# Performance work log

Measured on AMD Instinct MI355X. Metric: run time of the kernel, lower is better.

The kernel has to match this reference:

```python
import jax, jax.numpy as jnp
import numpy as np

H = 51  # hidden size hardcoded in the module

def _lstm_cell(x, h, c, W_ih, W_hh, b_ih, b_hh):
    # PyTorch LSTMCell: gates ordered (i, f, g, o)
    z = x @ W_ih.T + h @ W_hh.T + b_ih + b_hh  # [B, 4H]
    i, f, g, o = jnp.split(z, 4, axis=-1)
    i = jax.nn.sigmoid(i)
    f = jax.nn.sigmoid(f)
    g = jnp.tanh(g)
    o = jax.nn.sigmoid(o)
    c_new = f * c + i * g
    h_new = o * jnp.tanh(c_new)
    return h_new, c_new

def setup_inputs() -> dict:
    key = jax.random.key(0)
    ks = jax.random.split(key, 12)
    B, T = 512, 512
    s = 1.0 / np.sqrt(H)  # PyTorch default init scale
    def u(k, shape):
        return jax.random.uniform(k, shape, jnp.float32, -s, s)
    return {
        "input": jax.random.normal(ks[0], (B, T), jnp.float32),
        "W_ih1": u(ks[1], (4 * H, 1)),
        "W_hh1": u(ks[2], (4 * H, H)),
        "b_ih1": u(ks[3], (4 * H,)),
        "b_hh1": u(ks[4], (4 * H,)),
        "W_ih2": u(ks[5], (4 * H, H)),
        "W_hh2": u(ks[6], (4 * H, H)),
        "b_ih2": u(ks[7], (4 * H,)),
        "b_hh2": u(ks[8], (4 * H,)),
        "W_lin": u(ks[9], (1, H)),
        "b_lin": u(ks[10], (1,)),
        "future": 0,
    }

def reference(input, W_ih1, W_hh1, b_ih1, b_hh1, W_ih2, W_hh2, b_ih2, b_hh2, W_lin, b_lin, future):
    B, T = input.shape
    h1 = jnp.zeros((B, H), input.dtype)
    c1 = jnp.zeros((B, H), input.dtype)
    h2 = jnp.zeros((B, H), input.dtype)
    c2 = jnp.zeros((B, H), input.dtype)

    def step(carry, x_t):
        h1, c1, h2, c2 = carry
        h1, c1 = _lstm_cell(x_t, h1, c1, W_ih1, W_hh1, b_ih1, b_hh1)
        h2, c2 = _lstm_cell(h1, h2, c2, W_ih2, W_hh2, b_ih2, b_hh2)
        out = h2 @ W_lin.T + b_lin  # [B, 1]
        return (h1, c1, h2, c2), out

    xs = jnp.transpose(input)[:, :, None]  # [T, B, 1]
    carry, outs = jax.lax.scan(step, (h1, c1, h2, c2), xs)
    outputs = jnp.transpose(outs[:, :, 0])  # [B, T]

    if future > 0:
        last = outs[-1]  # [B, 1]

        def fstep(carry, _):
            state, x = carry
            state, out = step(state, x)
            return (state, out), out

        _, fouts = jax.lax.scan(fstep, (carry, last), None, length=future)
        outputs = jnp.concatenate([outputs, jnp.transpose(fouts[:, :, 0])], axis=1)
    return outputs
```

## Files before the change

### kernel.cpp

```cpp
#include <hip/hip_runtime.h>

#define Hh 51
#define TT 512
#define MR 2
#define NBLK 256
#define BT 512
#define SHR 80
#define NIT 514
#define LOG2E 1.4426950408889634f

typedef _Float16 half8 __attribute__((ext_vector_type(8)));
typedef __attribute__((ext_vector_type(4))) float f32x4;

__device__ __forceinline__ float fexp2(float x){ return __builtin_amdgcn_exp2f(x); }
__device__ __forceinline__ float frcp(float x){ return __builtin_amdgcn_rcpf(x); }
__device__ __forceinline__ float sigm(float x){ return frcp(1.f + fexp2(-LOG2E*x)); }
__device__ __forceinline__ float ftanh(float x){ return 1.f - 2.f*frcp(1.f + fexp2(2.f*LOG2E*x)); }
__device__ __forceinline__ unsigned short h16bits(_Float16 h){
    union { _Float16 h; unsigned short u; } c; c.h = h; return c.u;
}
__device__ __forceinline__ unsigned packhl(float v){
    _Float16 hi = (_Float16)v;
    _Float16 lo = (_Float16)(v - (float)hi);
    return (unsigned)h16bits(hi) | ((unsigned)h16bits(lo) << 16);
}

#define MFMAH(a,b,c) __builtin_amdgcn_mfma_f32_16x16x32_f16(a,b,c,0,0,0)

__global__ __launch_bounds__(BT, 2) void lstm2_fold(
    const float* __restrict__ input,
    const float* __restrict__ W_ih1,
    const float* __restrict__ W_hh1,
    const float* __restrict__ b_ih1,
    const float* __restrict__ b_hh1,
    const float* __restrict__ W_ih2,
    const float* __restrict__ W_hh2,
    const float* __restrict__ b_ih2,
    const float* __restrict__ b_hh2,
    const float* __restrict__ W_lin,
    const float* __restrict__ b_lin,
    float* __restrict__ out)
{
    __shared__ unsigned xsp[(TT+1)*MR];
    __shared__ float ob[TT*MR];
    __shared__ __align__(16) _Float16 H1[2][16*SHR];
    __shared__ __align__(16) _Float16 H2[2][16*SHR];

    const int tid  = threadIdx.x;
    const int wv   = tid >> 6;
    const int lane = tid & 63;
    const int quad = lane >> 4;
    const int n16  = lane & 15;
    const int row0 = blockIdx.x * MR;
    const bool g1  = (wv < 4);
    const bool w3  = (wv == 3);
    const int  w   = g1 ? wv : (wv - 4);
    const int  l   = 13 * w + n16;
    const bool valid = (n16 <= 12) && (l < Hh);
    const bool liveA = ((n16 & 11) == 0);
    const bool updL  = (quad < MR) && valid;
    const bool xw    = (wv == 0) && (n16 == 0) && (quad < MR);
    const int  fo    = n16 * SHR + quad * 8;
    const int  ho    = (quad * 4) * SHR + l;

#pragma unroll
    for (int i = 0; i < MR; ++i) {
        int idx = i * BT + tid; int m = idx >> 9, t = idx & 511;
        xsp[t * MR + m] = packhl(input[(row0 + m) * TT + t]);
    }
    if (tid < MR) xsp[TT * MR + tid] = 0u;
    for (int i = tid; i < 2 * 16 * SHR / 2; i += BT) {
        ((int*)H1)[i] = 0; ((int*)H2)[i] = 0;
    }

    half8 z8 = {0,0,0,0,0,0,0,0};
    half8 B1[4][2];
    half8 B2[4][2], B3[4][2];
    half8 Bout[2];
    const f32x4 zc = (f32x4){0.f,0.f,0.f,0.f};
#pragma unroll
    for (int gt = 0; gt < 4; ++gt) {
        int jrow = gt * Hh + l;
        float bias = 0.f, wih = 0.f;
        if (valid) {
            bias = g1 ? (b_ih1[jrow] + b_hh1[jrow]) : (b_ih2[jrow] + b_hh2[jrow]);
            wih  = g1 ? W_ih1[jrow] : 0.f;
        }
        _Float16 bhi = (_Float16)bias;
        _Float16 blo = (_Float16)(bias - (float)bhi);
        _Float16 wih_h = (_Float16)wih;
#pragma unroll
        for (int kt = 0; kt < 2; ++kt) {
            B1[gt][kt] = z8; B2[gt][kt] = z8; B3[gt][kt] = z8;
#pragma unroll
            for (int jj = 0; jj < 8; ++jj) {
                int k = kt * 32 + quad * 8 + jj;
                if (valid) {
                    if (g1) {
                        if (k < Hh)       B1[gt][kt][jj] = (_Float16)W_hh1[jrow * Hh + k];
                        else if (k == 51) B1[gt][kt][jj] = bhi;
                        else if (k == 52 || k == 53) B1[gt][kt][jj] = wih_h;
                        else if (k == 54) B1[gt][kt][jj] = blo;
                    } else {
                        if (k < Hh) {
                            B2[gt][kt][jj] = (_Float16)W_ih2[jrow * Hh + k];
                            B3[gt][kt][jj] = (_Float16)W_hh2[jrow * Hh + k];
                        } else if (k == 51) B2[gt][kt][jj] = bhi;
                        else if (k == 54)   B2[gt][kt][jj] = blo;
                    }
                }
            }
        }
    }
    {
        float blf = b_lin[0];
        _Float16 blhi = (_Float16)blf;
        _Float16 bllo = (_Float16)(blf - (float)blhi);
#pragma unroll
        for (int kt = 0; kt < 2; ++kt) {
            Bout[kt] = z8;
#pragma unroll
            for (int jj = 0; jj < 8; ++jj) {
                int k = kt * 32 + quad * 8 + jj;
                if (w3 && n16 == 0) {
                    if (k < Hh)       Bout[kt][jj] = (_Float16)W_lin[k];
                    else if (k == 51) Bout[kt][jj] = blhi;
                    else if (k == 54) Bout[kt][jj] = bllo;
                }
            }
        }
    }
    float cst = 0.f;

    half8 f1a = z8, f1b = z8;
    half8 f2a = z8, f2b = z8;

    __syncthreads();
    if (tid < MR) {
        int r = tid * 4 * SHR;
        const unsigned one = (unsigned)h16bits((_Float16)1.0f);
#pragma unroll
        for (int p = 0; p < 2; ++p) {
            H1[p][r + 51] = (_Float16)1.0f;  H1[p][r + 54] = (_Float16)1.0f;
            H2[p][r + 51] = (_Float16)1.0f;  H2[p][r + 54] = (_Float16)1.0f;
        }
        *(unsigned*)&H1[1][r + 52] = xsp[tid];
        (void)one;
    }
    __syncthreads();

    auto stepfn = [&](int n, int pA, int pB) {
        if (g1) {
            if (w3 && n >= 2) {
                if (liveA) {
                    f2a = *(const half8*)&H2[pB][fo];
                    f2b = *(const half8*)&H2[pB][fo + 32];
                }
            }
            if (n < TT) {
                unsigned xn = xw ? xsp[(n + 1) * MR + quad] : 0u;
                if (liveA) {
                    f1a = *(const half8*)&H1[pA][fo];
                    f1b = *(const half8*)&H1[pA][fo + 32];
                }
                f32x4 ac[4];
#pragma unroll
                for (int gt = 0; gt < 4; ++gt) {
                    f32x4 a = MFMAH(f1a, B1[gt][0], zc);
                    a       = MFMAH(f1b, B1[gt][1], a);
                    ac[gt] = a;
                }
                if (updL) {
                    float ii = sigm(ac[0][0]), ff = sigm(ac[1][0]);
                    float gg = ftanh(ac[2][0]), oo = sigm(ac[3][0]);
                    cst = fmaf(ff, cst, ii * gg);
                    float h = oo * ftanh(cst);
                    H1[pB][ho] = (_Float16)h;
                }
                if (xw) *(unsigned*)&H1[pB][(quad * 4) * SHR + 52] = xn;
            }
            if (w3 && n >= 2) {
                f32x4 ao = MFMAH(f2a, Bout[0], zc);
                ao       = MFMAH(f2b, Bout[1], ao);
                if (n16 == 0 && quad < MR) ob[(n - 2) * MR + quad] = ao[0];
            }
        } else if (n >= 1 && n <= TT) {
            if (liveA) {
                f1a = *(const half8*)&H1[pA][fo];
                f1b = *(const half8*)&H1[pA][fo + 32];
                f2a = *(const half8*)&H2[pB][fo];
                f2b = *(const half8*)&H2[pB][fo + 32];
            }
            f32x4 ac[4];
#pragma unroll
            for (int gt = 0; gt < 4; ++gt) {
                f32x4 a = MFMAH(f2a, B3[gt][0], zc);
                a       = MFMAH(f2b, B3[gt][1], a);
                a       = MFMAH(f1a, B2[gt][0], a);
                a       = MFMAH(f1b, B2[gt][1], a);
                ac[gt] = a;
            }
            if (updL) {
                float ii = sigm(ac[0][0]), ff = sigm(ac[1][0]);
                float gg = ftanh(ac[2][0]), oo = sigm(ac[3][0]);
                cst = fmaf(ff, cst, ii * gg);
                float h = oo * ftanh(cst);
                H2[pA][ho] = (_Float16)h;
            }
        }
        __syncthreads();
    };

    for (int k2 = 0; k2 < NIT / 2; ++k2) {
        stepfn(2 * k2,     1, 0);
        stepfn(2 * k2 + 1, 0, 1);
    }

#pragma unroll
    for (int i = 0; i < MR; ++i) {
        int idx = i * BT + tid; int m = idx >> 9, t = idx & 511;
        out[(row0 + m) * TT + t] = ob[t * MR + m];
    }
}

extern "C" void kernel_launch(void* const* d_in, const int* in_sizes, int n_in,
                              void* d_out, int out_size, void* d_ws, size_t ws_size,
                              hipStream_t stream) {
    const float* input = (const float*)d_in[0];
    const float* W_ih1 = (const float*)d_in[1];
    const float* W_hh1 = (const float*)d_in[2];
    const float* b_ih1 = (const float*)d_in[3];
    const float* b_hh1 = (const float*)d_in[4];
    const float* W_ih2 = (const float*)d_in[5];
    const float* W_hh2 = (const float*)d_in[6];
    const float* b_ih2 = (const float*)d_in[7];
    const float* b_hh2 = (const float*)d_in[8];
    const float* W_lin = (const float*)d_in[9];
    const float* b_lin = (const float*)d_in[10];
    float* out = (float*)d_out;

    hipLaunchKernelGGL(lstm2_fold, dim3(NBLK), dim3(BT), 0, stream,
                       input, W_ih1, W_hh1, b_ih1, b_hh1,
                       W_ih2, W_hh2, b_ih2, b_hh2, W_lin, b_lin, out);
}
```

Baseline: 272.0 us.

## Deepen LSTM wavefront pipeline to four stages with split MFMA chains

Expands the shared hidden-state buffers from double to quad buffering and skews the schedule. The second layer's input-weight product on h1 is computed one step early from a prefetched copy, and the output projection is lagged an extra step. Long dependent MFMA accumulation chains are split into independent MFMAs whose results are summed in scalar registers, which shortens the per-step critical path between barriers. The cost is two extra pipeline iterations, more shared memory and more live registers, which may hurt occupancy under the 2-blocks-per-CU launch bound.

```diff
diff --git a/kernel.cpp b/kernel.cpp
--- a/kernel.cpp
+++ b/kernel.cpp
@@ -6,7 +6,7 @@
 #define NBLK 256
 #define BT 512
 #define SHR 80
-#define NIT 514
+#define NIT 516
 #define LOG2E 1.4426950408889634f
 
 typedef _Float16 half8 __attribute__((ext_vector_type(8)));
@@ -43,8 +43,8 @@
 {
     __shared__ unsigned xsp[(TT+1)*MR];
     __shared__ float ob[TT*MR];
-    __shared__ __align__(16) _Float16 H1[2][16*SHR];
-    __shared__ __align__(16) _Float16 H2[2][16*SHR];
+    __shared__ __align__(16) _Float16 H1[4][16*SHR];
+    __shared__ __align__(16) _Float16 H2[4][16*SHR];
 
     const int tid  = threadIdx.x;
     const int wv   = tid >> 6;
@@ -69,7 +69,7 @@
         xsp[t * MR + m] = packhl(input[(row0 + m) * TT + t]);
     }
     if (tid < MR) xsp[TT * MR + tid] = 0u;
-    for (int i = tid; i < 2 * 16 * SHR / 2; i += BT) {
+    for (int i = tid; i < 4 * 16 * SHR / 2; i += BT) {
         ((int*)H1)[i] = 0; ((int*)H2)[i] = 0;
     }
 
@@ -134,86 +134,109 @@
 
     half8 f1a = z8, f1b = z8;
     half8 f2a = z8, f2b = z8;
+    half8 pf1a = z8, pf1b = z8;
+    half8 of2a = z8, of2b = z8;
 
     __syncthreads();
     if (tid < MR) {
         int r = tid * 4 * SHR;
-        const unsigned one = (unsigned)h16bits((_Float16)1.0f);
-#pragma unroll
-        for (int p = 0; p < 2; ++p) {
+#pragma unroll
+        for (int p = 0; p < 4; ++p) {
             H1[p][r + 51] = (_Float16)1.0f;  H1[p][r + 54] = (_Float16)1.0f;
             H2[p][r + 51] = (_Float16)1.0f;  H2[p][r + 54] = (_Float16)1.0f;
         }
-        *(unsigned*)&H1[1][r + 52] = xsp[tid];
-        (void)one;
+        *(unsigned*)&H1[3][r + 52] = xsp[tid];
     }
     __syncthreads();
 
-    auto stepfn = [&](int n, int pA, int pB) {
+    auto stepfn = [&](int n, int P) {
+        const int Sr1 = (P + 3) & 3;
+        const int Sw1 = P;
+        const int Sr2 = (P + 1) & 3;
+        const int Sw2 = (P + 2) & 3;
         if (g1) {
-            if (w3 && n >= 2) {
-                if (liveA) {
-                    f2a = *(const half8*)&H2[pB][fo];
-                    f2b = *(const half8*)&H2[pB][fo + 32];
-                }
-            }
             if (n < TT) {
                 unsigned xn = xw ? xsp[(n + 1) * MR + quad] : 0u;
                 if (liveA) {
-                    f1a = *(const half8*)&H1[pA][fo];
-                    f1b = *(const half8*)&H1[pA][fo + 32];
-                }
-                f32x4 ac[4];
+                    f1a = *(const half8*)&H1[Sr1][fo];
+                    f1b = *(const half8*)&H1[Sr1][fo + 32];
+                }
+                if (w3) {
+                    if (n >= 4) {
+                        f32x4 ao = MFMAH(of2a, Bout[0], zc);
+                        ao       = MFMAH(of2b, Bout[1], ao);
+                        if (n16 == 0 && quad < MR) ob[(n - 4) * MR + quad] = ao[0];
+                    }
+                    if (liveA) {
+                        of2a = *(const half8*)&H2[Sr2][fo];
+                        of2b = *(const half8*)&H2[Sr2][fo + 32];
+                    }
+                }
+                float vg[4];
 #pragma unroll
                 for (int gt = 0; gt < 4; ++gt) {
-                    f32x4 a = MFMAH(f1a, B1[gt][0], zc);
-                    a       = MFMAH(f1b, B1[gt][1], a);
-                    ac[gt] = a;
+                    f32x4 m1 = MFMAH(f1a, B1[gt][0], zc);
+                    f32x4 m2 = MFMAH(f1b, B1[gt][1], zc);
+                    vg[gt] = m1[0] + m2[0];
                 }
                 if (updL) {
-                    float ii = sigm(ac[0][0]), ff = sigm(ac[1][0]);
-                    float gg = ftanh(ac[2][0]), oo = sigm(ac[3][0]);
+                    float ii = sigm(vg[0]), ff = sigm(vg[1]);
+                    float gg = ftanh(vg[2]), oo = sigm(vg[3]);
                     cst = fmaf(ff, cst, ii * gg);
                     float h = oo * ftanh(cst);
-                    H1[pB][ho] = (_Float16)h;
-                }
-                if (xw) *(unsigned*)&H1[pB][(quad * 4) * SHR + 52] = xn;
-            }
-            if (w3 && n >= 2) {
-                f32x4 ao = MFMAH(f2a, Bout[0], zc);
-                ao       = MFMAH(f2b, Bout[1], ao);
-                if (n16 == 0 && quad < MR) ob[(n - 2) * MR + quad] = ao[0];
-            }
-        } else if (n >= 1 && n <= TT) {
+                    H1[Sw1][ho] = (_Float16)h;
+                }
+                if (xw) *(unsigned*)&H1[Sw1][(quad * 4) * SHR + 52] = xn;
+            } else if (w3) {
+                f32x4 ao = MFMAH(of2a, Bout[0], zc);
+                ao       = MFMAH(of2b, Bout[1], ao);
+                if (n16 == 0 && quad < MR) ob[(n - 4) * MR + quad] = ao[0];
+                if (liveA) {
+                    of2a = *(const half8*)&H2[Sr2][fo];
+                    of2b = *(const half8*)&H2[Sr2][fo + 32];
+                }
+            }
+        } else {
             if (liveA) {
-                f1a = *(const half8*)&H1[pA][fo];
-                f1b = *(const half8*)&H1[pA][fo + 32];
-                f2a = *(const half8*)&H2[pB][fo];
-                f2b = *(const half8*)&H2[pB][fo + 32];
-            }
-            f32x4 ac[4];
+                f2a = *(const half8*)&H2[Sr2][fo];
+                f2b = *(const half8*)&H2[Sr2][fo + 32];
+            }
+            f32x4 aB[4];
 #pragma unroll
             for (int gt = 0; gt < 4; ++gt) {
-                f32x4 a = MFMAH(f2a, B3[gt][0], zc);
-                a       = MFMAH(f2b, B3[gt][1], a);
-                a       = MFMAH(f1a, B2[gt][0], a);
-                a       = MFMAH(f1b, B2[gt][1], a);
-                ac[gt] = a;
-            }
-            if (updL) {
-                float ii = sigm(ac[0][0]), ff = sigm(ac[1][0]);
-                float gg = ftanh(ac[2][0]), oo = sigm(ac[3][0]);
-                cst = fmaf(ff, cst, ii * gg);
-                float h = oo * ftanh(cst);
-                H2[pA][ho] = (_Float16)h;
+                f32x4 a = MFMAH(pf1a, B2[gt][0], zc);
+                aB[gt]  = MFMAH(pf1b, B2[gt][1], a);
+            }
+            if (liveA) {
+                pf1a = *(const half8*)&H1[Sr1][fo];
+                pf1b = *(const half8*)&H1[Sr1][fo + 32];
+            }
+            if (n >= 2 && n < TT + 2) {
+                float vg[4];
+#pragma unroll
+                for (int gt = 0; gt < 4; ++gt) {
+                    f32x4 m1 = MFMAH(f2a, B3[gt][0], zc);
+                    f32x4 m2 = MFMAH(f2b, B3[gt][1], zc);
+                    vg[gt] = m1[0] + m2[0] + aB[gt][0];
+                }
+                if (updL) {
+                    float ii = sigm(vg[0]), ff = sigm(vg[1]);
+                    float gg = ftanh(vg[2]), oo = sigm(vg[3]);
+                    cst = fmaf(ff, cst, ii * gg);
+                    float h = oo * ftanh(cst);
+                    H2[Sw2][ho] = (_Float16)h;
+                }
             }
         }
         __syncthreads();
     };
 
-    for (int k2 = 0; k2 < NIT / 2; ++k2) {
-        stepfn(2 * k2,     1, 0);
-        stepfn(2 * k2 + 1, 0, 1);
+    for (int k4 = 0; k4 < NIT / 4; ++k4) {
+        int b = 4 * k4;
+        stepfn(b + 0, 0);
+        stepfn(b + 1, 1);
+        stepfn(b + 2, 2);
+        stepfn(b + 3, 3);
     }
 
 #pragma unroll
```

Result: slower. 285.2 us (+4.9%).

## Fold activation scales into weights and merge LSTM gate math with fewer reciprocals

Applied to the files above, without the earlier changes.

Pre-scales the LSTM weights and biases by -log2(e) or 2*log2(e) per gate, so the MFMA outputs feed exp2 directly without a multiply. The gate nonlinearities and cell update are rewritten algebraically, combining the sigmoid and tanh denominators so each step needs two reciprocals instead of five. Layer 2's four-MFMA dependent chain is split into two independent two-MFMA chains that are summed, shortening the latency on the serial recurrence path. The cost is extra multiplies and a clamp against overflow of the combined exp terms, plus a small change in fp16 rounding of the pre-scaled weights.

```diff
diff --git a/kernel.cpp b/kernel.cpp
--- a/kernel.cpp
+++ b/kernel.cpp
@@ -14,8 +14,6 @@
 
 __device__ __forceinline__ float fexp2(float x){ return __builtin_amdgcn_exp2f(x); }
 __device__ __forceinline__ float frcp(float x){ return __builtin_amdgcn_rcpf(x); }
-__device__ __forceinline__ float sigm(float x){ return frcp(1.f + fexp2(-LOG2E*x)); }
-__device__ __forceinline__ float ftanh(float x){ return 1.f - 2.f*frcp(1.f + fexp2(2.f*LOG2E*x)); }
 __device__ __forceinline__ unsigned short h16bits(_Float16 h){
     union { _Float16 h; unsigned short u; } c; c.h = h; return c.u;
 }
@@ -23,6 +21,24 @@
     _Float16 hi = (_Float16)v;
     _Float16 lo = (_Float16)(v - (float)hi);
     return (unsigned)h16bits(hi) | ((unsigned)h16bits(lo) << 16);
+}
+
+__device__ __forceinline__ float lstm_update(float vg0, float vg1, float vg2,
+                                             float vg3, float& cst){
+    float e_i = fexp2(vg0);
+    float e_f = fexp2(vg1);
+    float e_g = fexp2(vg2);
+    float e_o = fexp2(vg3);
+    float a_i = e_i + 1.f, a_f = e_f + 1.f;
+    float gp  = e_g + 1.f, gm = e_g - 1.f, a_o = e_o + 1.f;
+    float u  = a_i * gp;
+    float N  = fmaf(cst, u, gm * a_f);
+    float rD = frcp(a_f * u);
+    cst = N * rD;
+    float zc2 = fminf(2.f * LOG2E * cst, 60.f);
+    float e_c = fexp2(zc2);
+    float r2  = frcp((e_c + 1.f) * a_o);
+    return (e_c - 1.f) * r2;
 }
 
 #define MFMAH(a,b,c) __builtin_amdgcn_mfma_f32_16x16x32_f16(a,b,c,0,0,0)
@@ -80,11 +96,12 @@
     const f32x4 zc = (f32x4){0.f,0.f,0.f,0.f};
 #pragma unroll
     for (int gt = 0; gt < 4; ++gt) {
+        const float gs = (gt == 2) ? (2.f * LOG2E) : (-LOG2E);
         int jrow = gt * Hh + l;
         float bias = 0.f, wih = 0.f;
         if (valid) {
-            bias = g1 ? (b_ih1[jrow] + b_hh1[jrow]) : (b_ih2[jrow] + b_hh2[jrow]);
-            wih  = g1 ? W_ih1[jrow] : 0.f;
+            bias = gs * (g1 ? (b_ih1[jrow] + b_hh1[jrow]) : (b_ih2[jrow] + b_hh2[jrow]));
+            wih  = g1 ? (gs * W_ih1[jrow]) : 0.f;
         }
         _Float16 bhi = (_Float16)bias;
         _Float16 blo = (_Float16)(bias - (float)bhi);
@@ -97,14 +114,14 @@
                 int k = kt * 32 + quad * 8 + jj;
                 if (valid) {
                     if (g1) {
-                        if (k < Hh)       B1[gt][kt][jj] = (_Float16)W_hh1[jrow * Hh + k];
+                        if (k < Hh)       B1[gt][kt][jj] = (_Float16)(gs * W_hh1[jrow * Hh + k]);
                         else if (k == 51) B1[gt][kt][jj] = bhi;
                         else if (k == 52 || k == 53) B1[gt][kt][jj] = wih_h;
                         else if (k == 54) B1[gt][kt][jj] = blo;
                     } else {
                         if (k < Hh) {
-                            B2[gt][kt][jj] = (_Float16)W_ih2[jrow * Hh + k];
-                            B3[gt][kt][jj] = (_Float16)W_hh2[jrow * Hh + k];
+                            B2[gt][kt][jj] = (_Float16)(gs * W_ih2[jrow * Hh + k]);
+                            B3[gt][kt][jj] = (_Float16)(gs * W_hh2[jrow * Hh + k]);
                         } else if (k == 51) B2[gt][kt][jj] = bhi;
                         else if (k == 54)   B2[gt][kt][jj] = blo;
                     }
@@ -138,14 +155,12 @@
     __syncthreads();
     if (tid < MR) {
         int r = tid * 4 * SHR;
-        const unsigned one = (unsigned)h16bits((_Float16)1.0f);
 #pragma unroll
         for (int p = 0; p < 2; ++p) {
             H1[p][r + 51] = (_Float16)1.0f;  H1[p][r + 54] = (_Float16)1.0f;
             H2[p][r + 51] = (_Float16)1.0f;  H2[p][r + 54] = (_Float16)1.0f;
         }
         *(unsigned*)&H1[1][r + 52] = xsp[tid];
-        (void)one;
     }
     __syncthreads();
 
@@ -171,10 +186,7 @@
                     ac[gt] = a;
                 }
                 if (updL) {
-                    float ii = sigm(ac[0][0]), ff = sigm(ac[1][0]);
-                    float gg = ftanh(ac[2][0]), oo = sigm(ac[3][0]);
-                    cst = fmaf(ff, cst, ii * gg);
-                    float h = oo * ftanh(cst);
+                    float h = lstm_update(ac[0][0], ac[1][0], ac[2][0], ac[3][0], cst);
                     H1[pB][ho] = (_Float16)h;
                 }
                 if (xw) *(unsigned*)&H1[pB][(quad * 4) * SHR + 52] = xn;
@@ -191,20 +203,17 @@
                 f2a = *(const half8*)&H2[pB][fo];
                 f2b = *(const half8*)&H2[pB][fo + 32];
             }
-            f32x4 ac[4];
+            float vg[4];
 #pragma unroll
             for (int gt = 0; gt < 4; ++gt) {
-                f32x4 a = MFMAH(f2a, B3[gt][0], zc);
-                a       = MFMAH(f2b, B3[gt][1], a);
-                a       = MFMAH(f1a, B2[gt][0], a);
-                a       = MFMAH(f1b, B2[gt][1], a);
-                ac[gt] = a;
+                f32x4 m2 = MFMAH(f2a, B3[gt][0], zc);
+                m2       = MFMAH(f2b, B3[gt][1], m2);
+                f32x4 m1 = MFMAH(f1a, B2[gt][0], zc);
+                m1       = MFMAH(f1b, B2[gt][1], m1);
+                vg[gt] = m2[0] + m1[0];
             }
             if (updL) {
-                float ii = sigm(ac[0][0]), ff = sigm(ac[1][0]);
-                float gg = ftanh(ac[2][0]), oo = sigm(ac[3][0]);
-                cst = fmaf(ff, cst, ii * gg);
-                float h = oo * ftanh(cst);
+                float h = lstm_update(vg[0], vg[1], vg[2], vg[3], cst);
                 H2[pA][ho] = (_Float16)h;
             }
         }
```

New measurement: 280.8 us. 3.2% more time.
